# Kernel tuning notes

Measured on AMD Instinct MI355X. Metric: run time of the kernel, lower is better.

The kernel has to match this reference:

```python
import jax, jax.numpy as jnp
import numpy as np

HID = 64      # RNN hidden size (fixed in source)
K = 3         # B-spline order (pykan default)
NUM = 5       # grid intervals (pykan default)
DIMS = [64, 16, 1]  # layer_nums_small_nobi


def make_grid(in_dim):
    # uniform grid on [-1,1] extended by K knots each side -> NUM+2K+1 = 12 knots
    h = 2.0 / NUM
    g = jnp.arange(-K, NUM + K + 1, dtype=jnp.float32) * h - 1.0
    return jnp.broadcast_to(g, (in_dim, g.shape[0]))


def bspline_basis(x, grid):
    # x: (b, in), grid: (in, G) -> basis (b, in, G-K-1) via Cox-de Boor
    xe = x[..., None]
    B = ((xe >= grid[:, :-1]) & (xe < grid[:, 1:])).astype(x.dtype)
    for d in range(1, K + 1):
        left = (xe - grid[:, :-(d + 1)]) / (grid[:, d:-1] - grid[:, :-(d + 1)]) * B[..., :-1]
        right = (grid[:, d + 1:] - xe) / (grid[:, d + 1:] - grid[:, 1:-d]) * B[..., 1:]
        B = left + right
    return B  # (b, in, NUM+K)


def kan_layer(x, grid, coef, sb, sp):
    # coef: (in, out, NUM+K); sb, sp: (in, out)
    bas = bspline_basis(x, grid)                      # (b, in, NUM+K)
    spl = jnp.einsum('bik,iok->bio', bas, coef)       # per-edge spline value
    return jnp.einsum('bi,io->bo', jax.nn.silu(x), sb) + jnp.einsum('bio,io->bo', spl, sp)


def rnn_layer(x, w_ih, w_hh, b_ih, b_hh, return_seq):
    # x: (b, t, f), tanh RNN, h0 = 0
    h0 = jnp.zeros((x.shape[0], HID), x.dtype)
    def step(h, xt):
        h = jnp.tanh(xt @ w_ih.T + h @ w_hh.T + b_ih + b_hh)
        return h, (h if return_seq else 0.0)
    hT, ys = jax.lax.scan(step, h0, jnp.swapaxes(x, 0, 1))
    return jnp.swapaxes(ys, 0, 1) if return_seq else hT


def setup_inputs() -> dict:
    key = jax.random.key(0)
    ks = jax.random.split(key, 16)
    Bsz, T, F = 2048, 256, 64
    s = 1.0 / np.sqrt(HID)
    inp = {'x': jax.random.normal(ks[0], (Bsz, T, F), jnp.float32)}
    inp['w_ih0'] = jax.random.uniform(ks[1], (HID, F), jnp.float32, -s, s)
    inp['w_hh0'] = jax.random.uniform(ks[2], (HID, HID), jnp.float32, -s, s)
    inp['b_ih0'] = jax.random.uniform(ks[3], (HID,), jnp.float32, -s, s)
    inp['b_hh0'] = jax.random.uniform(ks[4], (HID,), jnp.float32, -s, s)
    inp['w_ih1'] = jax.random.uniform(ks[5], (HID, HID), jnp.float32, -s, s)
    inp['w_hh1'] = jax.random.uniform(ks[6], (HID, HID), jnp.float32, -s, s)
    inp['b_ih1'] = jax.random.uniform(ks[7], (HID,), jnp.float32, -s, s)
    inp['b_hh1'] = jax.random.uniform(ks[8], (HID,), jnp.float32, -s, s)
    kk = 9
    for i, (di, do) in enumerate(zip(DIMS[:-1], DIMS[1:])):
        inp[f'grid{i}'] = make_grid(di)
        inp[f'coef{i}'] = 0.1 * jax.random.normal(ks[kk], (di, do, NUM + K), jnp.float32)
        inp[f'sb{i}'] = (1.0 / np.sqrt(di)) * jnp.ones((di, do), jnp.float32) + 0.05 * jax.random.normal(ks[kk + 1], (di, do), jnp.float32)
        inp[f'sp{i}'] = jnp.ones((di, do), jnp.float32)
        kk += 2
    return inp


def reference(x, w_ih0, w_hh0, b_ih0, b_hh0, w_ih1, w_hh1, b_ih1, b_hh1,
              grid0, coef0, sb0, sp0, grid1, coef1, sb1, sp1):
    h1 = rnn_layer(x, w_ih0, w_hh0, b_ih0, b_hh0, return_seq=True)   # (b,t,64)
    out = rnn_layer(h1, w_ih1, w_hh1, b_ih1, b_hh1, return_seq=False)  # last step only
    out = kan_layer(out, grid0, coef0, sb0, sp0)   # (b,16)
    out = kan_layer(out, grid1, coef1, sb1, sp1)   # (b,1)
    return jnp.squeeze(jax.nn.sigmoid(out), 1)     # (b,)
```

## Files before the change

kernel.cpp:

```cpp
#include <hip/hip_runtime.h>
#include <cstdint>
#include <cstddef>

typedef __attribute__((ext_vector_type(8))) __bf16 bf16x8;
typedef __attribute__((ext_vector_type(4))) float f32x4;

#define MFMA16(a, b, c) __builtin_amdgcn_mfma_f32_16x16x32_bf16((a), (b), (c), 0, 0, 0)

__device__ __forceinline__ float fast_tanh(float z) {
    float e = __expf(2.0f * z);
    return 1.0f - 2.0f * __builtin_amdgcn_rcpf(e + 1.0f);
}
__device__ __forceinline__ float fast_sigmoid(float z) {
    return __builtin_amdgcn_rcpf(1.0f + __expf(-z));
}

__device__ __forceinline__ unsigned pk2(float a, float b) {
    union { __bf16 h[2]; unsigned u; } p;
    p.h[0] = (__bf16)a;
    p.h[1] = (__bf16)b;
    return p.u;
}

__device__ __forceinline__ bf16x8 cvt8(float4 a, float4 b) {
    bf16x8 f;
    f[0] = (__bf16)a.x; f[1] = (__bf16)a.y; f[2] = (__bf16)a.z; f[3] = (__bf16)a.w;
    f[4] = (__bf16)b.x; f[5] = (__bf16)b.y; f[6] = (__bf16)b.z; f[7] = (__bf16)b.w;
    return f;
}

__device__ __forceinline__ bf16x8 ldwfrag(const float* __restrict__ W, int row, int k0) {
    const float4 a = *(const float4*)(W + row * 64 + k0);
    const float4 b = *(const float4*)(W + row * 64 + k0 + 4);
    bf16x8 f;
    f[0] = (__bf16)a.x; f[1] = (__bf16)a.y; f[2] = (__bf16)a.z; f[3] = (__bf16)a.w;
    f[4] = (__bf16)b.x; f[5] = (__bf16)b.y; f[6] = (__bf16)b.z; f[7] = (__bf16)b.w;
    return f;
}

__device__ __forceinline__ void bspl8(float x, const float* kn, float* B) {
    float b[11];
#pragma unroll
    for (int m = 0; m < 11; ++m)
        b[m] = (x >= kn[m] && x < kn[m + 1]) ? 1.0f : 0.0f;
#pragma unroll
    for (int d = 1; d <= 3; ++d) {
#pragma unroll
        for (int m = 0; m + d < 11; ++m) {
            float lf = (x - kn[m]) / (kn[m + d] - kn[m]) * b[m];
            float rt = (kn[m + d + 1] - x) / (kn[m + d + 1] - kn[m + 1]) * b[m + 1];
            b[m] = lf + rt;
        }
    }
#pragma unroll
    for (int m = 0; m < 8; ++m) B[m] = b[m];
}

__global__ __launch_bounds__(256, 1) void rnn_kan_v4(
    const float* __restrict__ x,
    const float* __restrict__ wih0, const float* __restrict__ whh0,
    const float* __restrict__ bih0, const float* __restrict__ bhh0,
    const float* __restrict__ wih1, const float* __restrict__ whh1,
    const float* __restrict__ bih1, const float* __restrict__ bhh1,
    const float* __restrict__ grid0, const float* __restrict__ coef0,
    const float* __restrict__ sb0, const float* __restrict__ sp0,
    const float* __restrict__ grid1, const float* __restrict__ coef1,
    const float* __restrict__ sb1, const float* __restrict__ sp1,
    float* __restrict__ out)
{
    __shared__ __align__(16) unsigned char s_h1[2][2048];
    __shared__ __align__(16) unsigned char s_h2[2][2048];
    __shared__ __align__(16) float s_hf[16][68];
    __shared__ __align__(16) float s_bas[1024][12];
    __shared__ __align__(16) float s_e[16][17];

    const int tid  = threadIdx.x;
    const int wv   = tid >> 6;
    const int lane = tid & 63;
    const int sc   = lane & 15;
    const int gr   = lane >> 4;
    const int s0   = blockIdx.x << 4;

    const int wrow = 16 * wv + sc;
    const int kofs = 8 * gr;
    bf16x8 fWih0[2], fWhh0[2], fWih1[2], fWhh1[2];
#pragma unroll
    for (int kt = 0; kt < 2; ++kt) {
        fWih0[kt] = ldwfrag(wih0, wrow, 32 * kt + kofs);
        fWhh0[kt] = ldwfrag(whh0, wrow, 32 * kt + kofs);
        fWih1[kt] = ldwfrag(wih1, wrow, 32 * kt + kofs);
        fWhh1[kt] = ldwfrag(whh1, wrow, 32 * kt + kofs);
    }
    f32x4 b0v, b1v;
#pragma unroll
    for (int i = 0; i < 4; ++i) {
        const int h = 16 * wv + 4 * gr + i;
        b0v[i] = bih0[h] + bhh0[h];
        b1v[i] = bih1[h] + bhh1[h];
    }

    const unsigned swz  = (unsigned)(sc & 7) << 4;
    const unsigned offW  = sc * 128 + (((unsigned)(32 * wv + 8 * gr)) ^ swz);
    const unsigned offR0 = sc * 128 + (((unsigned)(16 * gr)) ^ swz);
    const unsigned offR1 = sc * 128 + (((unsigned)(64 + 16 * gr)) ^ swz);

    const float* xb = x + (size_t)(s0 + sc) * 16384 + kofs;

    float4 q0 = *(const float4*)(xb);      float4 q1 = *(const float4*)(xb + 4);
    float4 q2 = *(const float4*)(xb + 32); float4 q3 = *(const float4*)(xb + 36);
    float4 ra0 = *(const float4*)(xb + 64),  ra1 = *(const float4*)(xb + 68);
    float4 ra2 = *(const float4*)(xb + 96),  ra3 = *(const float4*)(xb + 100);
    float4 rb0 = *(const float4*)(xb + 128), rb1 = *(const float4*)(xb + 132);
    float4 rb2 = *(const float4*)(xb + 160), rb3 = *(const float4*)(xb + 164);

    f32x4 xz = MFMA16(fWih0[0], cvt8(q0, q1), b0v);
    xz = MFMA16(fWih0[1], cvt8(q2, q3), xz);

    {
        float v[4];
#pragma unroll
        for (int i = 0; i < 4; ++i) v[i] = fast_tanh(xz[i]);
        uint2 pw; pw.x = pk2(v[0], v[1]); pw.y = pk2(v[2], v[3]);
        *(uint2*)((char*)(&s_h1[0][0]) + offW) = pw;
    }
    xz = MFMA16(fWih0[0], cvt8(ra0, ra1), b0v);
    xz = MFMA16(fWih0[1], cvt8(ra2, ra3), xz);
    ra0 = rb0; ra1 = rb1; ra2 = rb2; ra3 = rb3;
    rb0 = *(const float4*)(xb + 192); rb1 = *(const float4*)(xb + 196);
    rb2 = *(const float4*)(xb + 224); rb3 = *(const float4*)(xb + 228);

    asm volatile("s_waitcnt lgkmcnt(0)" ::: "memory");
    __builtin_amdgcn_s_barrier();
    asm volatile("" ::: "memory");

    bf16x8 h1f0 = *(const bf16x8*)((const char*)(&s_h1[0][0]) + offR0);
    bf16x8 h1f1 = *(const bf16x8*)((const char*)(&s_h1[0][0]) + offR1);
    f32x4 h2z = b1v;

    for (int t = 1; t < 256; ++t) {
        const int par = t & 1;
        f32x4 z1 = MFMA16(fWhh0[0], h1f0, xz);
        z1 = MFMA16(fWhh0[1], h1f1, z1);
        f32x4 z2 = MFMA16(fWih1[0], h1f0, h2z);
        z2 = MFMA16(fWih1[1], h1f1, z2);

        float v1[4], v2[4];
#pragma unroll
        for (int i = 0; i < 4; ++i) v1[i] = fast_tanh(z1[i]);
        uint2 pw1; pw1.x = pk2(v1[0], v1[1]); pw1.y = pk2(v1[2], v1[3]);
        *(uint2*)((char*)(&s_h1[par][0]) + offW) = pw1;
#pragma unroll
        for (int i = 0; i < 4; ++i) v2[i] = fast_tanh(z2[i]);
        uint2 pw2; pw2.x = pk2(v2[0], v2[1]); pw2.y = pk2(v2[2], v2[3]);
        *(uint2*)((char*)(&s_h2[par][0]) + offW) = pw2;

        xz = MFMA16(fWih0[0], cvt8(ra0, ra1), b0v);
        xz = MFMA16(fWih0[1], cvt8(ra2, ra3), xz);
        ra0 = rb0; ra1 = rb1; ra2 = rb2; ra3 = rb3;
        {
            const float* pn = xb + (size_t)((t + 3 > 255) ? 255 : t + 3) * 64;
            rb0 = *(const float4*)(pn);      rb1 = *(const float4*)(pn + 4);
            rb2 = *(const float4*)(pn + 32); rb3 = *(const float4*)(pn + 36);
        }

        asm volatile("s_waitcnt lgkmcnt(0)" ::: "memory");
        __builtin_amdgcn_s_barrier();
        asm volatile("" ::: "memory");

        bf16x8 h2f0 = *(const bf16x8*)((const char*)(&s_h2[par][0]) + offR0);
        bf16x8 h2f1 = *(const bf16x8*)((const char*)(&s_h2[par][0]) + offR1);
        h1f0 = *(const bf16x8*)((const char*)(&s_h1[par][0]) + offR0);
        h1f1 = *(const bf16x8*)((const char*)(&s_h1[par][0]) + offR1);

        h2z = MFMA16(fWhh1[0], h2f0, b1v);
        h2z = MFMA16(fWhh1[1], h2f1, h2z);
    }

    {
        f32x4 z2 = MFMA16(fWih1[0], h1f0, h2z);
        z2 = MFMA16(fWih1[1], h1f1, z2);
        f32x4 hv;
#pragma unroll
        for (int i = 0; i < 4; ++i) hv[i] = fast_tanh(z2[i]);
        *(f32x4*)(&s_hf[sc][16 * wv + 4 * gr]) = hv;
    }
    __syncthreads();

    float kn0[12], kn1[12];
#pragma unroll
    for (int m = 0; m < 12; ++m) { kn0[m] = grid0[m]; kn1[m] = grid1[m]; }

    for (int q = tid; q < 1024; q += 256) {
        const int i = q >> 4, s = q & 15;
        const float v = s_hf[s][i];
        float B[8];
        bspl8(v, kn0, B);
        *(float4*)(&s_bas[q][0]) = make_float4(B[0], B[1], B[2], B[3]);
        *(float4*)(&s_bas[q][4]) = make_float4(B[4], B[5], B[6], B[7]);
        s_bas[q][8] = v * fast_sigmoid(v);
    }
    __syncthreads();

    {
        const int s = tid >> 4, o = tid & 15;
        float acc = 0.0f;
        for (int i = 0; i < 64; ++i) {
            const int q = (i << 4) + s;
            const float4 B0 = *(const float4*)(&s_bas[q][0]);
            const float4 B1 = *(const float4*)(&s_bas[q][4]);
            const float sil = s_bas[q][8];
            const float* cp = coef0 + i * 128 + o * 8;
            const float4 c0 = *(const float4*)cp;
            const float4 c1 = *(const float4*)(cp + 4);
            const float spl = B0.x * c0.x + B0.y * c0.y + B0.z * c0.z + B0.w * c0.w +
                              B1.x * c1.x + B1.y * c1.y + B1.z * c1.z + B1.w * c1.w;
            acc += sil * sb0[(i << 4) + o] + sp0[(i << 4) + o] * spl;
        }
        float B[8];
        bspl8(acc, kn1, B);
        const float* cp = coef1 + o * 8;
        float spl = 0.0f;
#pragma unroll
        for (int k = 0; k < 8; ++k) spl += B[k] * cp[k];
        s_e[s][o] = (acc * fast_sigmoid(acc)) * sb1[o] + sp1[o] * spl;
    }
    __syncthreads();

    if (tid < 16) {
        float sum = 0.0f;
#pragma unroll
        for (int o = 0; o < 16; ++o) sum += s_e[tid][o];
        out[s0 + tid] = fast_sigmoid(sum);
    }
}

extern "C" void kernel_launch(void* const* d_in, const int* in_sizes, int n_in,
                              void* d_out, int out_size, void* d_ws, size_t ws_size,
                              hipStream_t stream) {
    (void)n_in; (void)out_size; (void)d_ws; (void)ws_size;
    const int B = in_sizes[0] / (256 * 64);
    const int grid = B / 16;
    rnn_kan_v4<<<dim3(grid), dim3(256), 0, stream>>>(
        (const float*)d_in[0],
        (const float*)d_in[1], (const float*)d_in[2], (const float*)d_in[3], (const float*)d_in[4],
        (const float*)d_in[5], (const float*)d_in[6], (const float*)d_in[7], (const float*)d_in[8],
        (const float*)d_in[9], (const float*)d_in[10], (const float*)d_in[11], (const float*)d_in[12],
        (const float*)d_in[13], (const float*)d_in[14], (const float*)d_in[15], (const float*)d_in[16],
        (float*)d_out);
}
```

Baseline: 165.6 us.

## Split MFMA chains, deepen x prefetch ring, merge hidden buffers per step

Each recurrent MFMA pair is split into two independent accumulations that are summed afterwards. This shortens the dependent MFMA latency chain on the serial critical path. The x prefetch grows to a 3-slot register ring with a distance of four steps, and loads use explicit global address-space pointers. The two layers' hidden-state LDS buffers are merged into one double-buffered array, and the loop is unrolled by three so the slot indexing stays static, at the cost of more registers and extra vector adds.

```diff
diff --git a/kernel.cpp b/kernel.cpp
--- a/kernel.cpp
+++ b/kernel.cpp
@@ -13,6 +13,10 @@
 }
 __device__ __forceinline__ float fast_sigmoid(float z) {
     return __builtin_amdgcn_rcpf(1.0f + __expf(-z));
+}
+
+__device__ __forceinline__ f32x4 gload4(const float* p) {
+    return *(const __attribute__((address_space(1))) f32x4*)p;
 }
 
 __device__ __forceinline__ unsigned pk2(float a, float b) {
@@ -22,20 +26,17 @@
     return p.u;
 }
 
-__device__ __forceinline__ bf16x8 cvt8(float4 a, float4 b) {
+__device__ __forceinline__ bf16x8 cvt8(f32x4 a, f32x4 b) {
     bf16x8 f;
-    f[0] = (__bf16)a.x; f[1] = (__bf16)a.y; f[2] = (__bf16)a.z; f[3] = (__bf16)a.w;
-    f[4] = (__bf16)b.x; f[5] = (__bf16)b.y; f[6] = (__bf16)b.z; f[7] = (__bf16)b.w;
+    f[0] = (__bf16)a[0]; f[1] = (__bf16)a[1]; f[2] = (__bf16)a[2]; f[3] = (__bf16)a[3];
+    f[4] = (__bf16)b[0]; f[5] = (__bf16)b[1]; f[6] = (__bf16)b[2]; f[7] = (__bf16)b[3];
     return f;
 }
 
 __device__ __forceinline__ bf16x8 ldwfrag(const float* __restrict__ W, int row, int k0) {
-    const float4 a = *(const float4*)(W + row * 64 + k0);
-    const float4 b = *(const float4*)(W + row * 64 + k0 + 4);
-    bf16x8 f;
-    f[0] = (__bf16)a.x; f[1] = (__bf16)a.y; f[2] = (__bf16)a.z; f[3] = (__bf16)a.w;
-    f[4] = (__bf16)b.x; f[5] = (__bf16)b.y; f[6] = (__bf16)b.z; f[7] = (__bf16)b.w;
-    return f;
+    const f32x4 a = *(const f32x4*)(W + row * 64 + k0);
+    const f32x4 b = *(const f32x4*)(W + row * 64 + k0 + 4);
+    return cvt8(a, b);
 }
 
 __device__ __forceinline__ void bspl8(float x, const float* kn, float* B) {
@@ -56,7 +57,7 @@
     for (int m = 0; m < 8; ++m) B[m] = b[m];
 }
 
-__global__ __launch_bounds__(256, 1) void rnn_kan_v4(
+__global__ __launch_bounds__(256, 1) void rnn_kan_v6(
     const float* __restrict__ x,
     const float* __restrict__ wih0, const float* __restrict__ whh0,
     const float* __restrict__ bih0, const float* __restrict__ bhh0,
@@ -68,8 +69,7 @@
     const float* __restrict__ sb1, const float* __restrict__ sp1,
     float* __restrict__ out)
 {
-    __shared__ __align__(16) unsigned char s_h1[2][2048];
-    __shared__ __align__(16) unsigned char s_h2[2][2048];
+    __shared__ __align__(16) unsigned char s_h[2][4096];
     __shared__ __align__(16) float s_hf[16][68];
     __shared__ __align__(16) float s_bas[1024][12];
     __shared__ __align__(16) float s_e[16][17];
@@ -91,12 +91,13 @@
         fWih1[kt] = ldwfrag(wih1, wrow, 32 * kt + kofs);
         fWhh1[kt] = ldwfrag(whh1, wrow, 32 * kt + kofs);
     }
-    f32x4 b0v, b1v;
+    f32x4 b0v, b1v, zv;
 #pragma unroll
     for (int i = 0; i < 4; ++i) {
         const int h = 16 * wv + 4 * gr + i;
         b0v[i] = bih0[h] + bhh0[h];
         b1v[i] = bih1[h] + bhh1[h];
+        zv[i] = 0.0f;
     }
 
     const unsigned swz  = (unsigned)(sc & 7) << 4;
@@ -106,12 +107,17 @@
 
     const float* xb = x + (size_t)(s0 + sc) * 16384 + kofs;
 
-    float4 q0 = *(const float4*)(xb);      float4 q1 = *(const float4*)(xb + 4);
-    float4 q2 = *(const float4*)(xb + 32); float4 q3 = *(const float4*)(xb + 36);
-    float4 ra0 = *(const float4*)(xb + 64),  ra1 = *(const float4*)(xb + 68);
-    float4 ra2 = *(const float4*)(xb + 96),  ra3 = *(const float4*)(xb + 100);
-    float4 rb0 = *(const float4*)(xb + 128), rb1 = *(const float4*)(xb + 132);
-    float4 rb2 = *(const float4*)(xb + 160), rb3 = *(const float4*)(xb + 164);
+    f32x4 q0 = gload4(xb),        q1 = gload4(xb + 4);
+    f32x4 q2 = gload4(xb + 32),   q3 = gload4(xb + 36);
+    f32x4 p0 = gload4(xb + 64),   p1 = gload4(xb + 68);
+    f32x4 p2 = gload4(xb + 96),   p3 = gload4(xb + 100);
+    f32x4 r0[3], r1[3], r2[3], r3[3];
+#pragma unroll
+    for (int j = 0; j < 3; ++j) {
+        const float* pj = xb + (size_t)(2 + j) * 64;
+        r0[j] = gload4(pj);      r1[j] = gload4(pj + 4);
+        r2[j] = gload4(pj + 32); r3[j] = gload4(pj + 36);
+    }
 
     f32x4 xz = MFMA16(fWih0[0], cvt8(q0, q1), b0v);
     xz = MFMA16(fWih0[1], cvt8(q2, q3), xz);
@@ -121,64 +127,70 @@
 #pragma unroll
         for (int i = 0; i < 4; ++i) v[i] = fast_tanh(xz[i]);
         uint2 pw; pw.x = pk2(v[0], v[1]); pw.y = pk2(v[2], v[3]);
-        *(uint2*)((char*)(&s_h1[0][0]) + offW) = pw;
-    }
-    xz = MFMA16(fWih0[0], cvt8(ra0, ra1), b0v);
-    xz = MFMA16(fWih0[1], cvt8(ra2, ra3), xz);
-    ra0 = rb0; ra1 = rb1; ra2 = rb2; ra3 = rb3;
-    rb0 = *(const float4*)(xb + 192); rb1 = *(const float4*)(xb + 196);
-    rb2 = *(const float4*)(xb + 224); rb3 = *(const float4*)(xb + 228);
+        *(uint2*)((char*)(&s_h[0][0]) + offW) = pw;
+    }
+    *(uint2*)((char*)(&s_h[0][0]) + 2048 + offW) = make_uint2(0u, 0u);
+
+    xz = MFMA16(fWih0[0], cvt8(p0, p1), b0v);
+    xz = MFMA16(fWih0[1], cvt8(p2, p3), xz);
 
     asm volatile("s_waitcnt lgkmcnt(0)" ::: "memory");
     __builtin_amdgcn_s_barrier();
     asm volatile("" ::: "memory");
 
-    bf16x8 h1f0 = *(const bf16x8*)((const char*)(&s_h1[0][0]) + offR0);
-    bf16x8 h1f1 = *(const bf16x8*)((const char*)(&s_h1[0][0]) + offR1);
+    bf16x8 h1f0 = *(const bf16x8*)((const char*)(&s_h[0][0]) + offR0);
+    bf16x8 h1f1 = *(const bf16x8*)((const char*)(&s_h[0][0]) + offR1);
     f32x4 h2z = b1v;
 
+#pragma unroll 3
     for (int t = 1; t < 256; ++t) {
-        const int par = t & 1;
-        f32x4 z1 = MFMA16(fWhh0[0], h1f0, xz);
-        z1 = MFMA16(fWhh0[1], h1f1, z1);
-        f32x4 z2 = MFMA16(fWih1[0], h1f0, h2z);
-        z2 = MFMA16(fWih1[1], h1f1, z2);
-
-        float v1[4], v2[4];
+        const int slot = (t - 1) % 3;
+        char* hb = (char*)(&s_h[0][0]) + ((t & 1) << 12);
+
+        f32x4 z1a = MFMA16(fWhh0[0], h1f0, xz);
+        f32x4 z1b = MFMA16(fWhh0[1], h1f1, zv);
+        f32x4 z2a = MFMA16(fWih1[0], h1f0, h2z);
+        f32x4 z2b = MFMA16(fWih1[1], h1f1, zv);
+
+        f32x4 z1 = z1a + z1b;
+        float v1[4];
 #pragma unroll
         for (int i = 0; i < 4; ++i) v1[i] = fast_tanh(z1[i]);
         uint2 pw1; pw1.x = pk2(v1[0], v1[1]); pw1.y = pk2(v1[2], v1[3]);
-        *(uint2*)((char*)(&s_h1[par][0]) + offW) = pw1;
+        *(uint2*)(hb + offW) = pw1;
+
+        f32x4 z2 = z2a + z2b;
+        float v2[4];
 #pragma unroll
         for (int i = 0; i < 4; ++i) v2[i] = fast_tanh(z2[i]);
         uint2 pw2; pw2.x = pk2(v2[0], v2[1]); pw2.y = pk2(v2[2], v2[3]);
-        *(uint2*)((char*)(&s_h2[par][0]) + offW) = pw2;
-
-        xz = MFMA16(fWih0[0], cvt8(ra0, ra1), b0v);
-        xz = MFMA16(fWih0[1], cvt8(ra2, ra3), xz);
-        ra0 = rb0; ra1 = rb1; ra2 = rb2; ra3 = rb3;
+        *(uint2*)(hb + 2048 + offW) = pw2;
+
+        xz = MFMA16(fWih0[0], cvt8(r0[slot], r1[slot]), b0v);
+        xz = MFMA16(fWih0[1], cvt8(r2[slot], r3[slot]), xz);
         {
-            const float* pn = xb + (size_t)((t + 3 > 255) ? 255 : t + 3) * 64;
-            rb0 = *(const float4*)(pn);      rb1 = *(const float4*)(pn + 4);
-            rb2 = *(const float4*)(pn + 32); rb3 = *(const float4*)(pn + 36);
+            const float* pn = xb + (size_t)((t + 4 > 255) ? 255 : t + 4) * 64;
+            r0[slot] = gload4(pn);      r1[slot] = gload4(pn + 4);
+            r2[slot] = gload4(pn + 32); r3[slot] = gload4(pn + 36);
         }
 
         asm volatile("s_waitcnt lgkmcnt(0)" ::: "memory");
         __builtin_amdgcn_s_barrier();
         asm volatile("" ::: "memory");
 
-        bf16x8 h2f0 = *(const bf16x8*)((const char*)(&s_h2[par][0]) + offR0);
-        bf16x8 h2f1 = *(const bf16x8*)((const char*)(&s_h2[par][0]) + offR1);
-        h1f0 = *(const bf16x8*)((const char*)(&s_h1[par][0]) + offR0);
-        h1f1 = *(const bf16x8*)((const char*)(&s_h1[par][0]) + offR1);
+        h1f0 = *(const bf16x8*)(hb + offR0);
+        h1f1 = *(const bf16x8*)(hb + offR1);
+        bf16x8 h2f0 = *(const bf16x8*)(hb + 2048 + offR0);
+        bf16x8 h2f1 = *(const bf16x8*)(hb + 2048 + offR1);
 
         h2z = MFMA16(fWhh1[0], h2f0, b1v);
         h2z = MFMA16(fWhh1[1], h2f1, h2z);
     }
 
     {
-        f32x4 z2 = MFMA16(fWih1[0], h1f0, h2z);
-        z2 = MFMA16(fWih1[1], h1f1, z2);
+        f32x4 z2a = MFMA16(fWih1[0], h1f0, h2z);
+        f32x4 z2b = MFMA16(fWih1[1], h1f1, zv);
+        f32x4 z2 = z2a + z2b;
         f32x4 hv;
 #pragma unroll
         for (int i = 0; i < 4; ++i) hv[i] = fast_tanh(z2[i]);
@@ -240,7 +252,7 @@
     (void)n_in; (void)out_size; (void)d_ws; (void)ws_size;
     const int B = in_sizes[0] / (256 * 64);
     const int grid = B / 16;
-    rnn_kan_v4<<<dim3(grid), dim3(256), 0, stream>>>(
+    rnn_kan_v6<<<dim3(grid), dim3(256), 0, stream>>>(
         (const float*)d_in[0],
         (const float*)d_in[1], (const float*)d_in[2], (const float*)d_in[3], (const float*)d_in[4],
         (const float*)d_in[5], (const float*)d_in[6], (const float*)d_in[7], (const float*)d_in[8],
```

After: 146.5 us. -11.5%, faster.
